# Optimization experiments

Measured on AMD Instinct MI355X. Metric: run time of the kernel, lower is better.

## Reference

```python
import jax, jax.numpy as jnp
import numpy as np

B, N, T, F_IN, H, E_RAND = 4, 1024, 12, 64, 64, 32768


def _xavier_uniform(key, shape):
    fan_in, fan_out = shape[1], shape[0]
    a = np.sqrt(6.0 / (fan_in + fan_out)).astype(np.float32)
    return jax.random.uniform(key, shape, jnp.float32, -a, a)


def setup_inputs() -> dict:
    key = jax.random.key(0)
    ks = jax.random.split(key, 6)
    x = jax.random.normal(ks[0], (B, N, T, F_IN), jnp.float32)
    src = jax.random.randint(ks[1], (E_RAND,), 0, N)
    dst = jax.random.randint(ks[2], (E_RAND,), 0, N)
    loops = jnp.arange(N)  # self-loops: guarantee every softmax row is non-empty
    edge_index = jnp.stack([jnp.concatenate([src, loops]),
                            jnp.concatenate([dst, loops])]).astype(jnp.int64)
    W = _xavier_uniform(ks[3], (H, F_IN))        # nn.Linear weight layout [out, in]
    a_l = _xavier_uniform(ks[4], (H, 1))
    a_r = _xavier_uniform(ks[5], (H, 1))
    bias = jnp.zeros((H,), jnp.float32)
    return {"x": x, "edge_index": edge_index, "W": W, "a_l": a_l, "a_r": a_r, "bias": bias}


def reference(x, edge_index, W, a_l, a_r, bias):
    n = x.shape[1]
    x_in = x.transpose(0, 2, 1, 3)                       # [B,T,N,F_in]
    h = jnp.einsum('btnf,hf->btnh', x_in, W)             # [B,T,N,H]
    attn_l = h @ a_l                                     # [B,T,N,1]
    attn_r = h @ a_r                                     # [B,T,N,1]
    e = attn_l + attn_r.transpose(0, 1, 3, 2)            # [B,T,N,N]
    e = jnp.where(e >= 0, e, 0.2 * e)                    # leaky_relu(0.2)
    adj = jnp.zeros((n, n), dtype=bool).at[edge_index[0], edge_index[1]].set(True)
    e = jnp.where(adj, e, -jnp.inf)                      # mask non-edges
    alpha = jax.nn.softmax(e, axis=-1)                   # row softmax over neighbors
    out = jnp.einsum('btij,btjh->btih', alpha, h) + bias # aggregate
    out = out.transpose(0, 2, 1, 3)                      # back to [B,N,T,H]
    return jax.nn.gelu(out, approximate=False)
```

## Files before the change

### kernel.cpp

```cpp
#include <hip/hip_runtime.h>

#define NNODE 1024
#define TT 12
#define NBT 48
#define CAP 128
#define WORDS 32

__device__ __forceinline__ unsigned short f2bf(float f) {
    unsigned int u = __float_as_uint(f);
    u = (u + 0x7fffu + ((u >> 16) & 1u)) >> 16;
    return (unsigned short)u;
}
__device__ __forceinline__ float bf2f(unsigned int v) {
    return __uint_as_float(v << 16);
}


__global__ __launch_bounds__(256) void zero_bm(uint4* __restrict__ bm) {
    bm[blockIdx.x * 256 + threadIdx.x] = uint4{0, 0, 0, 0};
}


__global__ __launch_bounds__(256) void scatter_adj(const int* __restrict__ ei, int E,
                                                   unsigned int* __restrict__ bm) {
    int e = blockIdx.x * 256 + threadIdx.x;
    if (e < E) {
        int s = ei[e];
        int d = ei[E + e];
        atomicOr(&bm[s * WORDS + (d >> 5)], 1u << (d & 31));
    }
}


__global__ __launch_bounds__(256) void csr_and_h(const unsigned int* __restrict__ bm,
                                                 int* __restrict__ deg,
                                                 int* __restrict__ col,
                                                 const float* __restrict__ x,
                                                 const float* __restrict__ W,
                                                 const float* __restrict__ a_l,
                                                 const float* __restrict__ a_r,
                                                 unsigned short* __restrict__ hbuf,
                                                 float* __restrict__ al,
                                                 float* __restrict__ ar) {
    __shared__ float Wt[64 * 65];
    __shared__ float xs[4][8 * 64];
    int tid = threadIdx.x, w = tid >> 6, lane = tid & 63;
    int half = lane >> 5, sub = lane & 31;

    if (blockIdx.x < 128) {
        int i = blockIdx.x * 8 + w * 2 + half;
        unsigned int word = bm[i * WORDS + sub];
        int cnt = __popc(word);
        int incl = cnt;
        #pragma unroll
        for (int o = 1; o < 32; o <<= 1) {
            int tv = __shfl_up(incl, o, 32);
            if (sub >= o) incl += tv;
        }
        int total = __shfl(incl, 31, 32);
        int excl = incl - cnt;
        if (sub == 0) deg[i] = total;
        int* outp = col + i * CAP + excl;
        int idx = 0, base = sub * 32;
        while (word) {
            int b = __ffs(word) - 1;
            word &= word - 1;
            outp[idx++] = base + b;
        }
        return;
    }

    int bidx = blockIdx.x - 128;
    int bt = bidx >> 5;
    int n0 = (bidx & 31) * 32 + w * 8;
    int b = bt / TT, t = bt % TT;

    for (int idx = tid; idx < 4096; idx += 256) {
        int hh = idx >> 6, f = idx & 63;
        Wt[f * 65 + hh] = W[idx];
    }
    const float* xb = x + ((size_t)(b * NNODE + n0) * TT + t) * 64;
    #pragma unroll
    for (int r = 0; r < 8; r++)
        xs[w][r * 64 + lane] = xb[(size_t)r * TT * 64 + lane];
    __syncthreads();

    float acc[8] = {0, 0, 0, 0, 0, 0, 0, 0};
    #pragma unroll 16
    for (int f = 0; f < 64; f++) {
        float wv = Wt[f * 65 + lane];
        #pragma unroll
        for (int r = 0; r < 8; r++)
            acc[r] = fmaf(xs[w][r * 64 + f], wv, acc[r]);
    }

    float alc = a_l[lane], arc = a_r[lane];
    unsigned short* hb = hbuf + ((size_t)bt * NNODE + n0) * 64;
    #pragma unroll
    for (int r = 0; r < 8; r++) {
        hb[r * 64 + lane] = f2bf(acc[r]);
        float sl = acc[r] * alc, sr = acc[r] * arc;
        #pragma unroll
        for (int o = 32; o > 0; o >>= 1) {
            sl += __shfl_xor(sl, o);
            sr += __shfl_xor(sr, o);
        }
        if (lane == 0) {
            al[bt * NNODE + n0 + r] = sl;
            ar[bt * NNODE + n0 + r] = sr;
        }
    }
}


__global__ __launch_bounds__(384) void aggregate(const unsigned short* __restrict__ hbuf,
                                                 const float* __restrict__ al,
                                                 const float* __restrict__ ar,
                                                 const int* __restrict__ deg,
                                                 const int* __restrict__ col,
                                                 const float* __restrict__ bias,
                                                 float* __restrict__ out) {
    __shared__ int2 pl[6][CAP];
    int w = threadIdx.x >> 6, lane = threadIdx.x & 63;
    int half = lane >> 5, sub = lane & 31;
    int i = blockIdx.x >> 3;
    int g = blockIdx.x & 7;
    int bt = g * 6 + w;
    int b = bt / TT, t = bt % TT;

    int d = deg[i];
    const int* ci = col + i * CAP;
    float ali = al[bt * NNODE + i];
    const float* arb = ar + bt * NNODE;

    int c0 = 0, c1 = 0;
    float e0 = -1e30f, e1 = -1e30f;
    if (lane < d) {
        c0 = ci[lane];
        float e = ali + arb[c0];
        e0 = (e >= 0.f) ? e : 0.2f * e;
    }
    if (lane + 64 < d) {
        c1 = ci[lane + 64];
        float e = ali + arb[c1];
        e1 = (e >= 0.f) ? e : 0.2f * e;
    }
    float m = fmaxf(e0, e1);
    #pragma unroll
    for (int o = 32; o > 0; o >>= 1) m = fmaxf(m, __shfl_xor(m, o));
    float p0 = (lane < d) ? __expf(e0 - m) : 0.f;
    float p1 = (lane + 64 < d) ? __expf(e1 - m) : 0.f;
    float s = p0 + p1;
    #pragma unroll
    for (int o = 32; o > 0; o >>= 1) s += __shfl_xor(s, o);
    if (lane < d) pl[w][lane] = make_int2(c0, __float_as_int(p0));
    if (lane + 64 < d) pl[w][lane + 64] = make_int2(c1, __float_as_int(p1));

    const unsigned short* hb = hbuf + (size_t)bt * NNODE * 64;
    float a0 = 0.f, a1 = 0.f;
    #pragma unroll 8
    for (int k = 0; k < d; k += 2) {
        int kk = k + half;
        int2 cp = (kk < d) ? pl[w][kk] : make_int2(0, 0);
        unsigned int hv = *(const unsigned int*)(hb + cp.x * 64 + 2 * sub);
        float pv = __int_as_float(cp.y);
        a0 = fmaf(pv, bf2f(hv & 0xffffu), a0);
        a1 = fmaf(pv, bf2f(hv >> 16), a1);
    }
    a0 += __shfl_xor(a0, 32);
    a1 += __shfl_xor(a1, 32);

    float inv = 1.f / s;
    float2 bb = ((const float2*)bias)[sub];
    float v0 = a0 * inv + bb.x;
    float v1 = a1 * inv + bb.y;
    float g0 = 0.5f * v0 * (1.f + erff(v0 * 0.70710678118654752f));
    float g1 = 0.5f * v1 * (1.f + erff(v1 * 0.70710678118654752f));
    if (half == 0) {
        float2* op = (float2*)(out + ((size_t)(b * NNODE + i) * TT + t) * 64);
        op[sub] = make_float2(g0, g1);
    }
}


extern "C" void kernel_launch(void* const* d_in, const int* in_sizes, int n_in,
                              void* d_out, int out_size, void* d_ws, size_t ws_size,
                              hipStream_t stream) {
    const float* x    = (const float*)d_in[0];
    const int*   ei   = (const int*)d_in[1];
    const float* W    = (const float*)d_in[2];
    const float* a_l  = (const float*)d_in[3];
    const float* a_r  = (const float*)d_in[4];
    const float* bias = (const float*)d_in[5];
    float* out = (float*)d_out;
    int E = in_sizes[1] / 2;

    char* ws = (char*)d_ws;
    unsigned int* bm = (unsigned int*)ws;
    int* deg = (int*)(ws + (128 << 10));
    int* col = (int*)(ws + (128 << 10) + 8192);
    unsigned short* hbuf = (unsigned short*)(ws + (1 << 20));
    float* al = (float*)(ws + (1 << 20) + (size_t)NBT * NNODE * 64 * 2);
    float* ar = al + NBT * NNODE;

    zero_bm<<<32, 256, 0, stream>>>((uint4*)bm);
    scatter_adj<<<(E + 255) / 256, 256, 0, stream>>>(ei, E, bm);
    csr_and_h<<<128 + NBT * 32, 256, 0, stream>>>(bm, deg, col, x, W, a_l, a_r, hbuf, al, ar);
    aggregate<<<NNODE * 8, 384, 0, stream>>>(hbuf, al, ar, deg, col, bias, out);
}
```

Baseline: 64.61 us.

## Fuse adjacency build into CSR blocks and use bf16 MFMA for projection

Drops the separate zero and scatter kernels. Each of 16 CSR blocks now scans every edge and builds a bitmap for its own 64 rows in shared memory with LDS atomics, which removes two launches and the global atomics. The projection h = xW now runs on MFMA 16x16x32 bf16 instructions with inputs converted to bf16 in registers, instead of scalar FMAs from LDS. The cost is that each CSR block reads the full edge list, x and W lose precision before the matmul, and the few CSR blocks may become the longest path.

After: 98.88 us. 53.0% more time.

```diff
diff --git a/kernel.cpp b/kernel.cpp
--- a/kernel.cpp
+++ b/kernel.cpp
@@ -5,34 +5,22 @@
 #define NBT 48
 #define CAP 128
 #define WORDS 32
-
-__device__ __forceinline__ unsigned short f2bf(float f) {
+#define CSRB 16
+
+typedef __attribute__((ext_vector_type(8))) short bf16x8;
+typedef __attribute__((ext_vector_type(4))) float f32x4;
+
+__device__ __forceinline__ short bfh(float f) {
     unsigned int u = __float_as_uint(f);
     u = (u + 0x7fffu + ((u >> 16) & 1u)) >> 16;
-    return (unsigned short)u;
+    return (short)u;
 }
 __device__ __forceinline__ float bf2f(unsigned int v) {
     return __uint_as_float(v << 16);
 }
 
 
-__global__ __launch_bounds__(256) void zero_bm(uint4* __restrict__ bm) {
-    bm[blockIdx.x * 256 + threadIdx.x] = uint4{0, 0, 0, 0};
-}
-
-
-__global__ __launch_bounds__(256) void scatter_adj(const int* __restrict__ ei, int E,
-                                                   unsigned int* __restrict__ bm) {
-    int e = blockIdx.x * 256 + threadIdx.x;
-    if (e < E) {
-        int s = ei[e];
-        int d = ei[E + e];
-        atomicOr(&bm[s * WORDS + (d >> 5)], 1u << (d & 31));
-    }
-}
-
-
-__global__ __launch_bounds__(256) void csr_and_h(const unsigned int* __restrict__ bm,
+__global__ __launch_bounds__(256) void csr_and_h(const int* __restrict__ ei, int E,
                                                  int* __restrict__ deg,
                                                  int* __restrict__ col,
                                                  const float* __restrict__ x,
@@ -42,73 +30,112 @@
                                                  unsigned short* __restrict__ hbuf,
                                                  float* __restrict__ al,
                                                  float* __restrict__ ar) {
-    __shared__ float Wt[64 * 65];
-    __shared__ float xs[4][8 * 64];
+    __shared__ char smem[16896];
     int tid = threadIdx.x, w = tid >> 6, lane = tid & 63;
-    int half = lane >> 5, sub = lane & 31;
-
-    if (blockIdx.x < 128) {
-        int i = blockIdx.x * 8 + w * 2 + half;
-        unsigned int word = bm[i * WORDS + sub];
-        int cnt = __popc(word);
-        int incl = cnt;
+
+    if (blockIdx.x < CSRB) {
+        unsigned int* lbm = (unsigned int*)smem;
+        for (int q = tid; q < 64 * WORDS; q += 256) lbm[q] = 0u;
+        __syncthreads();
+        int base = blockIdx.x * 64;
+        for (int e = tid; e < E; e += 256) {
+            int s = ei[e];
+            unsigned int r = (unsigned int)(s - base);
+            if (r < 64u) {
+                int d2 = ei[E + e];
+                atomicOr(&lbm[r * WORDS + (d2 >> 5)], 1u << (d2 & 31));
+            }
+        }
+        __syncthreads();
+        int half = lane >> 5, sub = lane & 31;
+        for (int rr = 0; rr < 8; rr++) {
+            int rloc = w * 16 + rr * 2 + half;
+            int i = base + rloc;
+            unsigned int word = lbm[rloc * WORDS + sub];
+            int cnt = __popc(word), incl = cnt;
+            #pragma unroll
+            for (int o = 1; o < 32; o <<= 1) {
+                int tv = __shfl_up(incl, o, 32);
+                if (sub >= o) incl += tv;
+            }
+            int total = __shfl(incl, 31, 32);
+            int excl = incl - cnt;
+            if (sub == 0) deg[i] = total;
+            int* outp = col + i * CAP + excl;
+            int idx = 0, nb = sub * 32;
+            while (word) { int bp = __ffs(word) - 1; word &= word - 1; outp[idx++] = nb + bp; }
+        }
+        return;
+    }
+
+    int pb = blockIdx.x - CSRB;
+    int bt = pb >> 4;
+    int n0 = (pb & 15) * 64 + w * 16;
+    int b = bt / TT, t = bt % TT;
+    int m = lane & 15, kb = lane >> 4;
+
+    const float* xr = x + ((size_t)(b * NNODE + n0 + m) * TT + t) * 64 + kb * 8;
+    float4 x0 = *(const float4*)xr;
+    float4 x1 = *(const float4*)(xr + 4);
+    float4 x2 = *(const float4*)(xr + 32);
+    float4 x3 = *(const float4*)(xr + 36);
+    bf16x8 af0, af1;
+    af0[0] = bfh(x0.x); af0[1] = bfh(x0.y); af0[2] = bfh(x0.z); af0[3] = bfh(x0.w);
+    af0[4] = bfh(x1.x); af0[5] = bfh(x1.y); af0[6] = bfh(x1.z); af0[7] = bfh(x1.w);
+    af1[0] = bfh(x2.x); af1[1] = bfh(x2.y); af1[2] = bfh(x2.z); af1[3] = bfh(x2.w);
+    af1[4] = bfh(x3.x); af1[5] = bfh(x3.y); af1[6] = bfh(x3.z); af1[7] = bfh(x3.w);
+
+    f32x4 acc[4];
+    float alv[4], arv[4];
+    #pragma unroll
+    for (int nt = 0; nt < 4; nt++) {
+        acc[nt] = (f32x4){0.f, 0.f, 0.f, 0.f};
+        const float* wr_ = W + (nt * 16 + m) * 64 + kb * 8;
+        float4 w0 = *(const float4*)wr_;
+        float4 w1 = *(const float4*)(wr_ + 4);
+        float4 w2 = *(const float4*)(wr_ + 32);
+        float4 w3 = *(const float4*)(wr_ + 36);
+        bf16x8 bf0, bf1;
+        bf0[0] = bfh(w0.x); bf0[1] = bfh(w0.y); bf0[2] = bfh(w0.z); bf0[3] = bfh(w0.w);
+        bf0[4] = bfh(w1.x); bf0[5] = bfh(w1.y); bf0[6] = bfh(w1.z); bf0[7] = bfh(w1.w);
+        bf1[0] = bfh(w2.x); bf1[1] = bfh(w2.y); bf1[2] = bfh(w2.z); bf1[3] = bfh(w2.w);
+        bf1[4] = bfh(w3.x); bf1[5] = bfh(w3.y); bf1[6] = bfh(w3.z); bf1[7] = bfh(w3.w);
+        acc[nt] = __builtin_amdgcn_mfma_f32_16x16x32_bf16(af0, bf0, acc[nt], 0, 0, 0);
+        acc[nt] = __builtin_amdgcn_mfma_f32_16x16x32_bf16(af1, bf1, acc[nt], 0, 0, 0);
+        alv[nt] = a_l[nt * 16 + m];
+        arv[nt] = a_r[nt * 16 + m];
+    }
+
+    #pragma unroll
+    for (int j = 0; j < 4; j++) {
+        float sl = acc[0][j] * alv[0] + acc[1][j] * alv[1] + acc[2][j] * alv[2] + acc[3][j] * alv[3];
+        float sr = acc[0][j] * arv[0] + acc[1][j] * arv[1] + acc[2][j] * arv[2] + acc[3][j] * arv[3];
         #pragma unroll
-        for (int o = 1; o < 32; o <<= 1) {
-            int tv = __shfl_up(incl, o, 32);
-            if (sub >= o) incl += tv;
-        }
-        int total = __shfl(incl, 31, 32);
-        int excl = incl - cnt;
-        if (sub == 0) deg[i] = total;
-        int* outp = col + i * CAP + excl;
-        int idx = 0, base = sub * 32;
-        while (word) {
-            int b = __ffs(word) - 1;
-            word &= word - 1;
-            outp[idx++] = base + b;
-        }
-        return;
-    }
-
-    int bidx = blockIdx.x - 128;
-    int bt = bidx >> 5;
-    int n0 = (bidx & 31) * 32 + w * 8;
-    int b = bt / TT, t = bt % TT;
-
-    for (int idx = tid; idx < 4096; idx += 256) {
-        int hh = idx >> 6, f = idx & 63;
-        Wt[f * 65 + hh] = W[idx];
-    }
-    const float* xb = x + ((size_t)(b * NNODE + n0) * TT + t) * 64;
-    #pragma unroll
-    for (int r = 0; r < 8; r++)
-        xs[w][r * 64 + lane] = xb[(size_t)r * TT * 64 + lane];
-    __syncthreads();
-
-    float acc[8] = {0, 0, 0, 0, 0, 0, 0, 0};
-    #pragma unroll 16
-    for (int f = 0; f < 64; f++) {
-        float wv = Wt[f * 65 + lane];
-        #pragma unroll
-        for (int r = 0; r < 8; r++)
-            acc[r] = fmaf(xs[w][r * 64 + f], wv, acc[r]);
-    }
-
-    float alc = a_l[lane], arc = a_r[lane];
-    unsigned short* hb = hbuf + ((size_t)bt * NNODE + n0) * 64;
-    #pragma unroll
-    for (int r = 0; r < 8; r++) {
-        hb[r * 64 + lane] = f2bf(acc[r]);
-        float sl = acc[r] * alc, sr = acc[r] * arc;
-        #pragma unroll
-        for (int o = 32; o > 0; o >>= 1) {
+        for (int o = 1; o < 16; o <<= 1) {
             sl += __shfl_xor(sl, o);
             sr += __shfl_xor(sr, o);
         }
-        if (lane == 0) {
-            al[bt * NNODE + n0 + r] = sl;
-            ar[bt * NNODE + n0 + r] = sr;
-        }
+        if (m == 0) {
+            int row = n0 + kb * 4 + j;
+            al[bt * NNODE + row] = sl;
+            ar[bt * NNODE + row] = sr;
+        }
+    }
+
+    unsigned short* ht = (unsigned short*)smem + (size_t)w * (16 * 66);
+    #pragma unroll
+    for (int nt = 0; nt < 4; nt++)
+        #pragma unroll
+        for (int j = 0; j < 4; j++)
+            ht[(kb * 4 + j) * 66 + nt * 16 + m] = (unsigned short)bfh(acc[nt][j]);
+    unsigned int* hb32 = (unsigned int*)(hbuf + ((size_t)bt * NNODE + n0) * 64);
+    int half = lane >> 5, sub = lane & 31;
+    #pragma unroll
+    for (int rr = 0; rr < 8; rr++) {
+        int row = rr * 2 + half;
+        unsigned int lo = ht[row * 66 + sub * 2];
+        unsigned int hi = ht[row * 66 + sub * 2 + 1];
+        hb32[row * 32 + sub] = (lo & 0xffffu) | (hi << 16);
     }
 }
 
@@ -196,15 +223,12 @@
     int E = in_sizes[1] / 2;
 
     char* ws = (char*)d_ws;
-    unsigned int* bm = (unsigned int*)ws;
-    int* deg = (int*)(ws + (128 << 10));
-    int* col = (int*)(ws + (128 << 10) + 8192);
-    unsigned short* hbuf = (unsigned short*)(ws + (1 << 20));
-    float* al = (float*)(ws + (1 << 20) + (size_t)NBT * NNODE * 64 * 2);
+    int* deg = (int*)ws;
+    int* col = (int*)(ws + 8192);
+    unsigned short* hbuf = (unsigned short*)(ws + 8192 + (512 << 10));
+    float* al = (float*)(ws + 8192 + (512 << 10) + (size_t)NBT * NNODE * 64 * 2);
     float* ar = al + NBT * NNODE;
 
-    zero_bm<<<32, 256, 0, stream>>>((uint4*)bm);
-    scatter_adj<<<(E + 255) / 256, 256, 0, stream>>>(ei, E, bm);
-    csr_and_h<<<128 + NBT * 32, 256, 0, stream>>>(bm, deg, col, x, W, a_l, a_r, hbuf, al, ar);
+    csr_and_h<<<CSRB + NBT * 16, 256, 0, stream>>>(ei, E, deg, col, x, W, a_l, a_r, hbuf, al, ar);
     aggregate<<<NNODE * 8, 384, 0, stream>>>(hbuf, al, ar, deg, col, bias, out);
 }
```
